# Kernel optimization log

Hardware: AMD Instinct MI355X
Metric: run time of the kernel (lower is better)

Reference implementation:

```python
import jax, jax.numpy as jnp
import numpy as np

NUM_GRAPHS = 64
GRAPH_SIZE = 1024   # nodes per graph (equal-sized graphs -> batched form of the per-graph loop)
PROJ_DIM = 64       # ProjectionHead output_dim default
TEMPERATURE = 0.5   # GRACE default


def setup_inputs() -> dict:
    key = jax.random.key(0)
    k1, k2 = jax.random.split(key)
    N = NUM_GRAPHS * GRAPH_SIZE
    z1 = jax.random.normal(k1, (N, PROJ_DIM), dtype=jnp.float32)
    z2 = jax.random.normal(k2, (N, PROJ_DIM), dtype=jnp.float32)
    # batch assignment: graph ids, sorted, equal-sized graphs
    batch = jnp.repeat(jnp.arange(NUM_GRAPHS, dtype=jnp.int64), GRAPH_SIZE)
    return {"z1": z1, "z2": z2, "batch": batch, "num_graphs": NUM_GRAPHS}


def _node_nt_xent(z1, z2, num_graphs, temperature):
    # z1, z2: [N, d] projected node embeddings; equal-sized graphs of G nodes.
    N, d = z1.shape
    G = N // num_graphs
    # F.normalize(dim=1)
    z1 = z1 / jnp.linalg.norm(z1, axis=1, keepdims=True)
    z2 = z2 / jnp.linalg.norm(z2, axis=1, keepdims=True)
    z1g = z1.reshape(num_graphs, G, d)  # [B, G, d]
    z2g = z2.reshape(num_graphs, G, d)
    inv_t = 1.0 / temperature
    # within-graph similarity matrices [B, G, G]
    sim12 = jnp.einsum('bid,bjd->bij', z1g, z2g) * inv_t
    sim11 = jnp.einsum('bid,bjd->bij', z1g, z1g) * inv_t
    # positive = diag(sim12)
    pos = jnp.einsum('bid,bid->bi', z1g, z2g) * inv_t  # [B, G]
    eye = jnp.eye(G, dtype=bool)
    neg12 = jnp.where(eye, -jnp.inf, sim12)
    neg11 = jnp.where(eye, -jnp.inf, sim11)
    # cross-entropy with label 0 on logits = [pos | neg12 | neg11]
    # = logsumexp(all logits) - pos  (done without materializing the concat)
    lse12 = jax.nn.logsumexp(neg12, axis=-1)  # [B, G]
    lse11 = jax.nn.logsumexp(neg11, axis=-1)
    lse = jax.nn.logsumexp(jnp.stack([pos, lse12, lse11], axis=-1), axis=-1)
    # sum_g mean_g * n_g / N  ==  global mean over nodes
    return jnp.mean(lse - pos)


def reference(z1, z2, batch, num_graphs):
    # batch is consistent with equal-sized, sorted graph ids (see setup_inputs);
    # the ragged per-graph python loop collapses to one batched computation.
    return _node_nt_xent(z1, z2, int(num_graphs), TEMPERATURE)
```

## Files before the change

### kernel.cpp

```cpp
#include <hip/hip_runtime.h>
#include <hip/hip_bf16.h>

#define N_NODES 65536
#define NUM_G   64
#define GSIZE   1024
#define DIM     64

using frag_ab = __attribute__((ext_vector_type(8))) short;
using f32x4   = __attribute__((ext_vector_type(4))) float;

__device__ __forceinline__ unsigned short f2bf(float x) {
    union { float f; unsigned int u; } v; v.f = x;
    unsigned int r = v.u + 0x7FFFu + ((v.u >> 16) & 1u);
    return (unsigned short)(r >> 16);
}

__global__ __launch_bounds__(256) void normalize_k(
    const float* __restrict__ z1, const float* __restrict__ z2,
    unsigned short* __restrict__ z1n, unsigned short* __restrict__ z2n,
    float* __restrict__ pos)
{
    int tid = threadIdx.x;
    int row = blockIdx.x * 16 + (tid >> 4);
    int l4  = tid & 15;
    float4 v1 = *((const float4*)(z1 + (size_t)row * DIM) + l4);
    float4 v2 = *((const float4*)(z2 + (size_t)row * DIM) + l4);
    float ss1 = v1.x*v1.x + v1.y*v1.y + v1.z*v1.z + v1.w*v1.w;
    float ss2 = v2.x*v2.x + v2.y*v2.y + v2.z*v2.z + v2.w*v2.w;
    float dt  = v1.x*v2.x + v1.y*v2.y + v1.z*v2.z + v1.w*v2.w;
    #pragma unroll
    for (int m = 1; m < 16; m <<= 1) {
        ss1 += __shfl_xor(ss1, m);
        ss2 += __shfl_xor(ss2, m);
        dt  += __shfl_xor(dt,  m);
    }
    float in1 = 1.0f / sqrtf(ss1);
    float in2 = 1.0f / sqrtf(ss2);
    ushort4 o1, o2;
    o1.x = f2bf(v1.x*in1); o1.y = f2bf(v1.y*in1); o1.z = f2bf(v1.z*in1); o1.w = f2bf(v1.w*in1);
    o2.x = f2bf(v2.x*in2); o2.y = f2bf(v2.y*in2); o2.z = f2bf(v2.z*in2); o2.w = f2bf(v2.w*in2);
    *((ushort4*)(z1n + (size_t)row * DIM) + l4) = o1;
    *((ushort4*)(z2n + (size_t)row * DIM) + l4) = o2;
    if (l4 == 0) pos[row] = dt * in1 * in2 * 2.0f;
}

__global__ __launch_bounds__(256, 2) void grace_main_k(
    const unsigned short* __restrict__ z1n,
    const unsigned short* __restrict__ z2n,
    const float* __restrict__ pos,
    float* __restrict__ partials)
{
    __shared__ unsigned short smem[2][64 * 64];
    __shared__ float red[4];

    int tid = threadIdx.x;
    int g = blockIdx.x >> 3, stripe = blockIdx.x & 7;
    int w = tid >> 6, l = tid & 63;
    const unsigned short* z1g = z1n + (size_t)g * GSIZE * DIM;
    const unsigned short* z2g = z2n + (size_t)g * GSIZE * DIM;
    int rowBase = stripe * 128 + w * 32;

    int ar = l & 15, ak = (l >> 4) * 8;
    frag_ab a00 = *(const frag_ab*)(z1g + (rowBase +  0 + ar) * DIM +  0 + ak);
    frag_ab a01 = *(const frag_ab*)(z1g + (rowBase +  0 + ar) * DIM + 32 + ak);
    frag_ab a10 = *(const frag_ab*)(z1g + (rowBase + 16 + ar) * DIM +  0 + ak);
    frag_ab a11 = *(const frag_ab*)(z1g + (rowBase + 16 + ar) * DIM + 32 + ak);

    float expacc[2][4] = {};

    int e0 = tid, e1 = tid + 256;
    int wcol0 = e0 >> 3, wslot0 = e0 & 7;
    int wcol1 = e1 >> 3, wslot1 = e1 & 7;
    int off0 = ((wcol0 << 7) + (wslot0 << 4)) ^ ((wcol0 & 7) << 4);
    int off1 = ((wcol1 << 7) + (wslot1 << 4)) ^ ((wcol1 & 7) << 4);

    auto src_ptr = [&](int p, int col, int slot) -> const int4* {
        const unsigned short* s = (p < 16) ? z2g : z1g;
        return (const int4*)(s + ((p & 15) * 64 + col) * DIM + slot * 8);
    };

    int bcol = l & 15, bgrp = l >> 4;

    int4 pre0 = *src_ptr(0, wcol0, wslot0);
    int4 pre1 = *src_ptr(0, wcol1, wslot1);
    *(int4*)((char*)smem[0] + off0) = pre0;
    *(int4*)((char*)smem[0] + off1) = pre1;
    pre0 = *src_ptr(1, wcol0, wslot0);
    pre1 = *src_ptr(1, wcol1, wslot1);
    __syncthreads();

    for (int p = 0; p < 32; ++p) {
        const char* base = (const char*)smem[p & 1];
        #pragma unroll
        for (int ct = 0; ct < 4; ++ct) {
            int col = ct * 16 + bcol;
            int boff0 = ((col << 7) + ((0 * 4 + bgrp) << 4)) ^ ((l & 7) << 4);
            int boff1 = ((col << 7) + ((1 * 4 + bgrp) << 4)) ^ ((l & 7) << 4);
            f32x4 zero = {0.f, 0.f, 0.f, 0.f};
            frag_ab b0 = *(const frag_ab*)(base + boff0);
            f32x4 c0 = __builtin_amdgcn_mfma_f32_16x16x32_bf16(a00, b0, zero, 0, 0, 0);
            f32x4 c1 = __builtin_amdgcn_mfma_f32_16x16x32_bf16(a10, b0, zero, 0, 0, 0);
            frag_ab b1 = *(const frag_ab*)(base + boff1);
            c0 = __builtin_amdgcn_mfma_f32_16x16x32_bf16(a01, b1, c0, 0, 0, 0);
            c1 = __builtin_amdgcn_mfma_f32_16x16x32_bf16(a11, b1, c1, 0, 0, 0);
            #pragma unroll
            for (int r = 0; r < 4; ++r) {
                expacc[0][r] += __expf(fmaf(c0[r], 2.0f, -2.0f));
                expacc[1][r] += __expf(fmaf(c1[r], 2.0f, -2.0f));
            }
        }
        if (p + 1 < 32) {
            char* wb = (char*)smem[(p + 1) & 1];
            *(int4*)(wb + off0) = pre0;
            *(int4*)(wb + off1) = pre1;
            if (p + 2 < 32) {
                pre0 = *src_ptr(p + 2, wcol0, wslot0);
                pre1 = *src_ptr(p + 2, wcol1, wslot1);
            }
            __syncthreads();
        }
    }

    float part = 0.f;
    #pragma unroll
    for (int t = 0; t < 2; ++t) {
        #pragma unroll
        for (int r = 0; r < 4; ++r) {
            float s = expacc[t][r];
            s += __shfl_xor(s, 1); s += __shfl_xor(s, 2);
            s += __shfl_xor(s, 4); s += __shfl_xor(s, 8);
            if ((l & 15) == 0) {
                int row = rowBase + t * 16 + (l >> 4) * 4 + r;
                int node = g * GSIZE + row;
                part += 2.0f + logf(s - 1.0f) - pos[node];
            }
        }
    }
    #pragma unroll
    for (int m = 1; m < 64; m <<= 1) part += __shfl_xor(part, m);
    if (l == 0) red[w] = part;
    __syncthreads();
    if (tid == 0) partials[blockIdx.x] = red[0] + red[1] + red[2] + red[3];
}

__global__ __launch_bounds__(256) void final_reduce_k(
    const float* __restrict__ partials, float* __restrict__ out)
{
    int tid = threadIdx.x;
    float s = partials[tid] + partials[tid + 256];
    #pragma unroll
    for (int m = 1; m < 64; m <<= 1) s += __shfl_xor(s, m);
    __shared__ float red[4];
    if ((tid & 63) == 0) red[tid >> 6] = s;
    __syncthreads();
    if (tid == 0) out[0] = (red[0] + red[1] + red[2] + red[3]) * (1.0f / N_NODES);
}

extern "C" void kernel_launch(void* const* d_in, const int* in_sizes, int n_in,
                              void* d_out, int out_size, void* d_ws, size_t ws_size,
                              hipStream_t stream)
{
    const float* z1 = (const float*)d_in[0];
    const float* z2 = (const float*)d_in[1];
    char* ws = (char*)d_ws;
    unsigned short* z1n = (unsigned short*)ws;
    unsigned short* z2n = (unsigned short*)(ws + 8388608);
    float* pos          = (float*)(ws + 16777216);
    float* partials     = (float*)(ws + 17039360);

    normalize_k<<<dim3(N_NODES / 16), dim3(256), 0, stream>>>(z1, z2, z1n, z2n, pos);
    grace_main_k<<<dim3(NUM_G * 8), dim3(256), 0, stream>>>(z1n, z2n, pos, partials);
    final_reduce_k<<<dim3(1), dim3(256), 0, stream>>>(partials, (float*)d_out);
}
```

Measured before the change: 47.34 us.

## Software-pipeline MFMA panels against exp accumulation of previous panel

Restructures the main loop into a two-panel ping-pong: each panel's MFMA results go into register arrays, and the exp accumulation of the previous panel runs while the next panel's matrix ops are issued. The aim is to overlap transcendental VALU work with MFMA latency. The exp is rewritten as exp2f with the log2(e) factor folded into the FMA constants, and the final log uses the fast __logf. In exchange it holds more accumulator registers live, which could reduce occupancy under the launch bound of 2, and the fast log is slightly less precise.

```diff
diff --git a/kernel.cpp b/kernel.cpp
--- a/kernel.cpp
+++ b/kernel.cpp
@@ -67,6 +67,7 @@
     frag_ab a11 = *(const frag_ab*)(z1g + (rowBase + 16 + ar) * DIM + 32 + ak);
 
     float expacc[2][4] = {};
+    f32x4 Ce[4][2], Co[4][2];
 
     int e0 = tid, e1 = tid + 256;
     int wcol0 = e0 >> 3, wslot0 = e0 & 7;
@@ -79,7 +80,37 @@
         return (const int4*)(s + ((p & 15) * 64 + col) * DIM + slot * 8);
     };
 
-    int bcol = l & 15, bgrp = l >> 4;
+    int bcol = l & 15, bgrp = l >> 4, bx = (l & 7) << 4;
+
+    auto panel_mfma = [&](f32x4 (&C)[4][2], const unsigned short* buf) {
+        const char* base = (const char*)buf;
+        #pragma unroll
+        for (int ct = 0; ct < 4; ++ct) {
+            int col = ct * 16 + bcol;
+            int boff0 = ((col << 7) + (bgrp << 4)) ^ bx;
+            int boff1 = ((col << 7) + ((4 + bgrp) << 4)) ^ bx;
+            frag_ab b0 = *(const frag_ab*)(base + boff0);
+            frag_ab b1 = *(const frag_ab*)(base + boff1);
+            f32x4 z = {0.f, 0.f, 0.f, 0.f};
+            f32x4 t0 = __builtin_amdgcn_mfma_f32_16x16x32_bf16(a00, b0, z, 0, 0, 0);
+            f32x4 t1 = __builtin_amdgcn_mfma_f32_16x16x32_bf16(a10, b0, z, 0, 0, 0);
+            C[ct][0] = __builtin_amdgcn_mfma_f32_16x16x32_bf16(a01, b1, t0, 0, 0, 0);
+            C[ct][1] = __builtin_amdgcn_mfma_f32_16x16x32_bf16(a11, b1, t1, 0, 0, 0);
+        }
+    };
+
+    const float K1 = 2.8853900817779268f;
+    const float K0 = -2.8853900817779268f;
+    auto acc_exp = [&](f32x4 (&C)[4][2]) {
+        #pragma unroll
+        for (int ct = 0; ct < 4; ++ct) {
+            #pragma unroll
+            for (int r = 0; r < 4; ++r) {
+                expacc[0][r] += exp2f(fmaf(C[ct][0][r], K1, K0));
+                expacc[1][r] += exp2f(fmaf(C[ct][1][r], K1, K0));
+            }
+        }
+    };
 
     int4 pre0 = *src_ptr(0, wcol0, wslot0);
     int4 pre1 = *src_ptr(0, wcol1, wslot1);
@@ -89,37 +120,28 @@
     pre1 = *src_ptr(1, wcol1, wslot1);
     __syncthreads();
 
-    for (int p = 0; p < 32; ++p) {
-        const char* base = (const char*)smem[p & 1];
-        #pragma unroll
-        for (int ct = 0; ct < 4; ++ct) {
-            int col = ct * 16 + bcol;
-            int boff0 = ((col << 7) + ((0 * 4 + bgrp) << 4)) ^ ((l & 7) << 4);
-            int boff1 = ((col << 7) + ((1 * 4 + bgrp) << 4)) ^ ((l & 7) << 4);
-            f32x4 zero = {0.f, 0.f, 0.f, 0.f};
-            frag_ab b0 = *(const frag_ab*)(base + boff0);
-            f32x4 c0 = __builtin_amdgcn_mfma_f32_16x16x32_bf16(a00, b0, zero, 0, 0, 0);
-            f32x4 c1 = __builtin_amdgcn_mfma_f32_16x16x32_bf16(a10, b0, zero, 0, 0, 0);
-            frag_ab b1 = *(const frag_ab*)(base + boff1);
-            c0 = __builtin_amdgcn_mfma_f32_16x16x32_bf16(a01, b1, c0, 0, 0, 0);
-            c1 = __builtin_amdgcn_mfma_f32_16x16x32_bf16(a11, b1, c1, 0, 0, 0);
-            #pragma unroll
-            for (int r = 0; r < 4; ++r) {
-                expacc[0][r] += __expf(fmaf(c0[r], 2.0f, -2.0f));
-                expacc[1][r] += __expf(fmaf(c1[r], 2.0f, -2.0f));
-            }
+    #pragma unroll 1
+    for (int i = 0; i < 16; ++i) {
+        panel_mfma(Ce, smem[0]);
+        *(int4*)((char*)smem[1] + off0) = pre0;
+        *(int4*)((char*)smem[1] + off1) = pre1;
+        if (i < 15) {
+            pre0 = *src_ptr(2 * i + 2, wcol0, wslot0);
+            pre1 = *src_ptr(2 * i + 2, wcol1, wslot1);
         }
-        if (p + 1 < 32) {
-            char* wb = (char*)smem[(p + 1) & 1];
-            *(int4*)(wb + off0) = pre0;
-            *(int4*)(wb + off1) = pre1;
-            if (p + 2 < 32) {
-                pre0 = *src_ptr(p + 2, wcol0, wslot0);
-                pre1 = *src_ptr(p + 2, wcol1, wslot1);
-            }
-            __syncthreads();
+        if (i > 0) acc_exp(Co);
+        __syncthreads();
+        panel_mfma(Co, smem[1]);
+        if (i < 15) {
+            *(int4*)((char*)smem[0] + off0) = pre0;
+            *(int4*)((char*)smem[0] + off1) = pre1;
+            pre0 = *src_ptr(2 * i + 3, wcol0, wslot0);
+            pre1 = *src_ptr(2 * i + 3, wcol1, wslot1);
         }
+        acc_exp(Ce);
+        if (i < 15) __syncthreads();
     }
+    acc_exp(Co);
 
     float part = 0.f;
     #pragma unroll
@@ -132,7 +154,7 @@
             if ((l & 15) == 0) {
                 int row = rowBase + t * 16 + (l >> 4) * 4 + r;
                 int node = g * GSIZE + row;
-                part += 2.0f + logf(s - 1.0f) - pos[node];
+                part += 2.0f + __logf(s - 1.0f) - pos[node];
             }
         }
     }
```

Measured after the change: 61.88 us. 1.31x slower.

## Restructure main kernel to 512 threads, 128-column tiles, exp2 and graph swizzle

Applied to the files above, without the earlier changes.

The main kernel now runs 8 waves per block, each owning 16 rows instead of 32, and stages 128 key columns per shared-memory tile, so there are 16 pipeline steps instead of 32. Block indices are remapped so neighbouring blocks work on different graphs, and the next tile's global prefetch is issued before compute. The exponent uses exp2 with a prescaled constant and a fast log. In exchange, each wave now reuses each B fragment for one MFMA row tile instead of two, and the larger block raises register and LDS pressure.

```diff
diff --git a/kernel.cpp b/kernel.cpp
--- a/kernel.cpp
+++ b/kernel.cpp
@@ -44,103 +44,100 @@
     if (l4 == 0) pos[row] = dt * in1 * in2 * 2.0f;
 }
 
-__global__ __launch_bounds__(256, 2) void grace_main_k(
+__global__ __launch_bounds__(512, 4) void grace_main_k(
     const unsigned short* __restrict__ z1n,
     const unsigned short* __restrict__ z2n,
     const float* __restrict__ pos,
     float* __restrict__ partials)
 {
-    __shared__ unsigned short smem[2][64 * 64];
-    __shared__ float red[4];
+    __shared__ unsigned short smem[2][128 * 64];
+    __shared__ float red[8];
 
     int tid = threadIdx.x;
-    int g = blockIdx.x >> 3, stripe = blockIdx.x & 7;
+    int n = blockIdx.x;
+    int g = (n & 7) + 8 * (n >> 6);
+    int stripe = (n >> 3) & 7;
     int w = tid >> 6, l = tid & 63;
     const unsigned short* z1g = z1n + (size_t)g * GSIZE * DIM;
     const unsigned short* z2g = z2n + (size_t)g * GSIZE * DIM;
-    int rowBase = stripe * 128 + w * 32;
+    int rowBase = stripe * 128 + w * 16;
 
     int ar = l & 15, ak = (l >> 4) * 8;
-    frag_ab a00 = *(const frag_ab*)(z1g + (rowBase +  0 + ar) * DIM +  0 + ak);
-    frag_ab a01 = *(const frag_ab*)(z1g + (rowBase +  0 + ar) * DIM + 32 + ak);
-    frag_ab a10 = *(const frag_ab*)(z1g + (rowBase + 16 + ar) * DIM +  0 + ak);
-    frag_ab a11 = *(const frag_ab*)(z1g + (rowBase + 16 + ar) * DIM + 32 + ak);
+    frag_ab a0 = *(const frag_ab*)(z1g + (rowBase + ar) * DIM +  0 + ak);
+    frag_ab a1 = *(const frag_ab*)(z1g + (rowBase + ar) * DIM + 32 + ak);
 
-    float expacc[2][4] = {};
+    float expacc[4] = {};
 
-    int e0 = tid, e1 = tid + 256;
-    int wcol0 = e0 >> 3, wslot0 = e0 & 7;
-    int wcol1 = e1 >> 3, wslot1 = e1 & 7;
-    int off0 = ((wcol0 << 7) + (wslot0 << 4)) ^ ((wcol0 & 7) << 4);
-    int off1 = ((wcol1 << 7) + (wslot1 << 4)) ^ ((wcol1 & 7) << 4);
+    int col0 = tid >> 3, slot = tid & 7;
+    int col1 = col0 + 64;
+    int off0 = ((col0 << 7) + (slot << 4)) ^ ((col0 & 7) << 4);
+    int off1 = ((col1 << 7) + (slot << 4)) ^ ((col1 & 7) << 4);
 
-    auto src_ptr = [&](int p, int col, int slot) -> const int4* {
-        const unsigned short* s = (p < 16) ? z2g : z1g;
-        return (const int4*)(s + ((p & 15) * 64 + col) * DIM + slot * 8);
+    auto src_ptr = [&](int p, int c) -> const int4* {
+        int j = p * 128 + c;
+        const unsigned short* s = (j < 1024) ? (z2g + j * DIM) : (z1g + (j - 1024) * DIM);
+        return (const int4*)(s + slot * 8);
     };
 
-    int bcol = l & 15, bgrp = l >> 4;
+    int bcol = l & 15, bgrp = l >> 4, bx = (l & 7) << 4;
 
-    int4 pre0 = *src_ptr(0, wcol0, wslot0);
-    int4 pre1 = *src_ptr(0, wcol1, wslot1);
+    const float K1 = 2.8853900817779268f;
+    const float K0 = -2.8853900817779268f;
+
+    int4 pre0 = *src_ptr(0, col0);
+    int4 pre1 = *src_ptr(0, col1);
     *(int4*)((char*)smem[0] + off0) = pre0;
     *(int4*)((char*)smem[0] + off1) = pre1;
-    pre0 = *src_ptr(1, wcol0, wslot0);
-    pre1 = *src_ptr(1, wcol1, wslot1);
     __syncthreads();
 
-    for (int p = 0; p < 32; ++p) {
-        const char* base = (const char*)smem[p & 1];
+    #pragma unroll 1
+    for (int i = 0; i < 16; ++i) {
+        if (i < 15) {
+            pre0 = *src_ptr(i + 1, col0);
+            pre1 = *src_ptr(i + 1, col1);
+        }
+        const char* base = (const char*)smem[i & 1];
         #pragma unroll
-        for (int ct = 0; ct < 4; ++ct) {
+        for (int ct = 0; ct < 8; ++ct) {
             int col = ct * 16 + bcol;
-            int boff0 = ((col << 7) + ((0 * 4 + bgrp) << 4)) ^ ((l & 7) << 4);
-            int boff1 = ((col << 7) + ((1 * 4 + bgrp) << 4)) ^ ((l & 7) << 4);
-            f32x4 zero = {0.f, 0.f, 0.f, 0.f};
-            frag_ab b0 = *(const frag_ab*)(base + boff0);
-            f32x4 c0 = __builtin_amdgcn_mfma_f32_16x16x32_bf16(a00, b0, zero, 0, 0, 0);
-            f32x4 c1 = __builtin_amdgcn_mfma_f32_16x16x32_bf16(a10, b0, zero, 0, 0, 0);
-            frag_ab b1 = *(const frag_ab*)(base + boff1);
-            c0 = __builtin_amdgcn_mfma_f32_16x16x32_bf16(a01, b1, c0, 0, 0, 0);
-            c1 = __builtin_amdgcn_mfma_f32_16x16x32_bf16(a11, b1, c1, 0, 0, 0);
+            frag_ab b0 = *(const frag_ab*)(base + (((col << 7) + (bgrp << 4)) ^ bx));
+            frag_ab b1 = *(const frag_ab*)(base + (((col << 7) + ((4 + bgrp) << 4)) ^ bx));
+            f32x4 z = {0.f, 0.f, 0.f, 0.f};
+            f32x4 c = __builtin_amdgcn_mfma_f32_16x16x32_bf16(a0, b0, z, 0, 0, 0);
+            c = __builtin_amdgcn_mfma_f32_16x16x32_bf16(a1, b1, c, 0, 0, 0);
             #pragma unroll
-            for (int r = 0; r < 4; ++r) {
-                expacc[0][r] += __expf(fmaf(c0[r], 2.0f, -2.0f));
-                expacc[1][r] += __expf(fmaf(c1[r], 2.0f, -2.0f));
-            }
+            for (int r = 0; r < 4; ++r)
+                expacc[r] += __builtin_amdgcn_exp2f(fmaf(c[r], K1, K0));
         }
-        if (p + 1 < 32) {
-            char* wb = (char*)smem[(p + 1) & 1];
+        if (i < 15) {
+            char* wb = (char*)smem[(i + 1) & 1];
             *(int4*)(wb + off0) = pre0;
             *(int4*)(wb + off1) = pre1;
-            if (p + 2 < 32) {
-                pre0 = *src_ptr(p + 2, wcol0, wslot0);
-                pre1 = *src_ptr(p + 2, wcol1, wslot1);
-            }
             __syncthreads();
         }
     }
 
     float part = 0.f;
     #pragma unroll
-    for (int t = 0; t < 2; ++t) {
-        #pragma unroll
-        for (int r = 0; r < 4; ++r) {
-            float s = expacc[t][r];
-            s += __shfl_xor(s, 1); s += __shfl_xor(s, 2);
-            s += __shfl_xor(s, 4); s += __shfl_xor(s, 8);
-            if ((l & 15) == 0) {
-                int row = rowBase + t * 16 + (l >> 4) * 4 + r;
-                int node = g * GSIZE + row;
-                part += 2.0f + logf(s - 1.0f) - pos[node];
-            }
+    for (int r = 0; r < 4; ++r) {
+        float s = expacc[r];
+        s += __shfl_xor(s, 1); s += __shfl_xor(s, 2);
+        s += __shfl_xor(s, 4); s += __shfl_xor(s, 8);
+        if ((l & 15) == 0) {
+            int row = rowBase + (l >> 4) * 4 + r;
+            part += 2.0f + __logf(s - 1.0f) - pos[g * GSIZE + row];
         }
     }
     #pragma unroll
     for (int m = 1; m < 64; m <<= 1) part += __shfl_xor(part, m);
     if (l == 0) red[w] = part;
     __syncthreads();
-    if (tid == 0) partials[blockIdx.x] = red[0] + red[1] + red[2] + red[3];
+    if (tid == 0) {
+        float s = 0.f;
+        #pragma unroll
+        for (int k = 0; k < 8; ++k) s += red[k];
+        partials[blockIdx.x] = s;
+    }
 }
 
 __global__ __launch_bounds__(256) void final_reduce_k(
@@ -169,6 +166,6 @@
     float* partials     = (float*)(ws + 17039360);
 
     normalize_k<<<dim3(N_NODES / 16), dim3(256), 0, stream>>>(z1, z2, z1n, z2n, pos);
-    grace_main_k<<<dim3(NUM_G * 8), dim3(256), 0, stream>>>(z1n, z2n, pos, partials);
+    grace_main_k<<<dim3(NUM_G * 8), dim3(512), 0, stream>>>(z1n, z2n, pos, partials);
     final_reduce_k<<<dim3(1), dim3(256), 0, stream>>>(partials, (float*)d_out);
 }
```

After: 45.48 us. 1.04x faster.
